# Kernel tuning notes

Hardware: AMD Instinct MI355X
Metric: run time of the kernel (lower is better)

## Reference

```python
import jax, jax.numpy as jnp
import numpy as np


def setup_inputs() -> dict:
    key = jax.random.key(0)
    k1, k2, k3, k4 = jax.random.split(key, 4)
    B, T, C = 4, 2048, 1024
    x = jax.random.normal(k1, (B, T, C), dtype=jnp.float32)
    scale = 1.0 / np.sqrt(C)
    Wq = jax.random.normal(k2, (C, C), dtype=jnp.float32) * scale
    Wk = jax.random.normal(k3, (C, C), dtype=jnp.float32) * scale
    Wv = jax.random.normal(k4, (C, C), dtype=jnp.float32) * scale
    return {"x": x, "Wq": Wq, "Wk": Wk, "Wv": Wv}


def reference(x, Wq, Wk, Wv):
    # x: [B, T, C]; torch Linear(no bias): y = x @ W.T
    B, T, C = x.shape
    q = jnp.einsum('btc,dc->btd', x, Wq)
    k = jnp.einsum('btc,dc->btd', x, Wk)
    v = jnp.einsum('btc,dc->btd', x, Wv)
    scale = jnp.asarray(C, x.dtype) ** -0.5
    qk = jnp.einsum('bqd,bkd->bqk', q, k) * scale  # [B, T, T]
    causal = jnp.tril(jnp.ones((T, T), dtype=bool))
    qk = jnp.where(causal, qk, -jnp.inf)
    attn = jax.nn.softmax(qk, axis=-1)
    out = jnp.einsum('bqk,bkd->bqd', attn, v)
    return out
```

## Files before the change

### kernel.cpp

```cpp
#include <hip/hip_runtime.h>

typedef __attribute__((ext_vector_type(8))) short  short8;
typedef __attribute__((ext_vector_type(4))) short  short4v;
typedef __attribute__((ext_vector_type(4))) float  floatx4;

__device__ inline short f2bf(float f) {
    union { float f; unsigned u; } v; v.f = f;
    unsigned r = v.u + 0x7fffu + ((v.u >> 16) & 1u);
    return (short)(r >> 16);
}

typedef const __attribute__((address_space(1))) unsigned int* gp1_t;
typedef __attribute__((address_space(3))) unsigned int* lp3_t;

__device__ __attribute__((always_inline)) inline void gl_lds16(const short* g, short* l) {
    __builtin_amdgcn_global_load_lds((gp1_t)g, (lp3_t)l, 16, 0, 0);
}

#define MFMA_BF16 __builtin_amdgcn_mfma_f32_16x16x32_bf16

__device__ __attribute__((always_inline)) inline void gemm_bt_core(
    const short* __restrict__ Ag, const short* __restrict__ Bg,
    int lda, int ldb, int kmax,
    short* As, short* Bs, floatx4 acc[4][4])
{
    const int t    = threadIdx.x;
    const int srow = t >> 3;
    const int scol = (t & 7) * 8;
    const int lane = t & 63;
    const int wid  = t >> 6;
    const int wx   = wid & 1, wy = wid >> 1;
    const int lm   = lane & 15, lq = lane >> 4;

    for (int k0 = 0; k0 < kmax; k0 += 64) {
        __syncthreads();
#pragma unroll
        for (int i = 0; i < 4; ++i) {
            gl_lds16(Ag + (size_t)(i * 32 + srow) * lda + k0 + scol,
                     As + (i * 32 + srow) * 64 + scol);
            gl_lds16(Bg + (size_t)(i * 32 + srow) * ldb + k0 + scol,
                     Bs + (i * 32 + srow) * 64 + scol);
        }
        __syncthreads();

#pragma unroll
        for (int ks = 0; ks < 2; ++ks) {
            short8 af[4], bfr[4];
#pragma unroll
            for (int mi = 0; mi < 4; ++mi)
                af[mi] = *(const short8*)(As + (wy * 64 + mi * 16 + lm) * 64 + ks * 32 + lq * 8);
#pragma unroll
            for (int ni = 0; ni < 4; ++ni)
                bfr[ni] = *(const short8*)(Bs + (wx * 64 + ni * 16 + lm) * 64 + ks * 32 + lq * 8);
#pragma unroll
            for (int mi = 0; mi < 4; ++mi)
#pragma unroll
                for (int ni = 0; ni < 4; ++ni)
                    acc[mi][ni] = MFMA_BF16(af[mi], bfr[ni], acc[mi][ni], 0, 0, 0);
        }
    }
}

__global__ void cast_all(const float* __restrict__ x,
                         const float* __restrict__ Wq,
                         const float* __restrict__ Wk,
                         const float* __restrict__ Wv,
                         short* __restrict__ xb, short* __restrict__ wb,
                         float* __restrict__ lsum)
{
    size_t v = (size_t)blockIdx.x * 256 + threadIdx.x;
    const float* src; short* dst; size_t off;
    if (v < 2097152)      { src = x;  dst = xb;           off = v; }
    else if (v < 2359296) { src = Wq; dst = wb;           off = v - 2097152; }
    else if (v < 2621440) { src = Wk; dst = wb + 1048576; off = v - 2359296; }
    else if (v < 2883584) { src = Wv; dst = wb + 2097152; off = v - 2621440; }
    else if (v < 2885632) {
        floatx4 z = {0.f, 0.f, 0.f, 0.f};
        ((floatx4*)lsum)[v - 2883584] = z;
        return;
    } else return;
    floatx4 vv = ((const floatx4*)src)[off];
    short4v s;
#pragma unroll
    for (int e = 0; e < 4; ++e) s[e] = f2bf(vv[e]);
    ((short4v*)dst)[off] = s;
}

__global__ __launch_bounds__(256, 3) void qkv_gemm(
    const short* __restrict__ xb, const short* __restrict__ wb,
    short* __restrict__ qb, short* __restrict__ kb, short* __restrict__ vt)
{
    __shared__ short As[128 * 64];
    __shared__ short Bs[128 * 64];

    const int m0    = blockIdx.x * 128;
    const int which = blockIdx.y >> 3;
    const int n0    = (blockIdx.y & 7) * 128;

    floatx4 acc[4][4];
    floatx4 zero = {0.f, 0.f, 0.f, 0.f};
#pragma unroll
    for (int i = 0; i < 4; ++i)
#pragma unroll
        for (int j = 0; j < 4; ++j) acc[i][j] = zero;

    gemm_bt_core(xb + (size_t)m0 * 1024,
                 wb + (size_t)blockIdx.y * 128 * 1024,
                 1024, 1024, 1024, As, Bs, acc);

    const int lane = threadIdx.x & 63, wid = threadIdx.x >> 6;
    const int wx = wid & 1, wy = wid >> 1, lm = lane & 15, lq = lane >> 4;
#pragma unroll
    for (int mi = 0; mi < 4; ++mi)
#pragma unroll
        for (int ni = 0; ni < 4; ++ni)
#pragma unroll
            for (int r = 0; r < 4; ++r) {
                int row = m0 + wy * 64 + mi * 16 + lq * 4 + r;
                int col = n0 + wx * 64 + ni * 16 + lm;
                short bvv = f2bf(acc[mi][ni][r]);
                if (which == 2) {
                    int bb = row >> 11, tt = row & 2047;
                    vt[((size_t)bb * 1024 + col) * 2048 + tt] = bvv;
                } else if (which == 1) {
                    kb[(size_t)row * 1024 + col] = bvv;
                } else {
                    qb[(size_t)row * 1024 + col] = bvv;
                }
            }
}

__global__ __launch_bounds__(256, 3) void sqk_gemm(
    const short* __restrict__ qb, const short* __restrict__ kb,
    short* __restrict__ P, float* __restrict__ lsum)
{
    int idx = blockIdx.x;
    int i = 0;
    while ((i + 1) * (i + 2) / 2 <= idx) ++i;
    const int j = idx - i * (i + 1) / 2;
    const int b = blockIdx.y;

    __shared__ short As[128 * 64];
    __shared__ short Bs[128 * 64];

    floatx4 acc[4][4];
    floatx4 zero = {0.f, 0.f, 0.f, 0.f};
#pragma unroll
    for (int a = 0; a < 4; ++a)
#pragma unroll
        for (int c = 0; c < 4; ++c) acc[a][c] = zero;

    gemm_bt_core(qb + ((size_t)(b * 2048 + i * 128)) * 1024,
                 kb + ((size_t)(b * 2048 + j * 128)) * 1024,
                 1024, 1024, 1024, As, Bs, acc);

    const float sscl = 0.03125f * 1.44269504089f;
    const bool  diag = (i == j);
    const int lane = threadIdx.x & 63, wid = threadIdx.x >> 6;
    const int wx = wid & 1, wy = wid >> 1, lm = lane & 15, lq = lane >> 4;

#pragma unroll
    for (int mi = 0; mi < 4; ++mi)
#pragma unroll
        for (int r = 0; r < 4; ++r) {
            const int lrow = wy * 64 + mi * 16 + lq * 4 + r;
            const int grow = i * 128 + lrow;
            short* prow = P + ((size_t)b * 2048 + grow) * 2048 + j * 128;
            float rsum = 0.f;
#pragma unroll
            for (int ni = 0; ni < 4; ++ni) {
                const int lcol = wx * 64 + ni * 16 + lm;
                float p = exp2f(acc[mi][ni][r] * sscl);
                if (diag && lcol > lrow) p = 0.f;
                rsum += p;
                prow[lcol] = f2bf(p);
            }
#pragma unroll
            for (int off = 1; off < 16; off <<= 1) rsum += __shfl_xor(rsum, off);
            if (lm == 0) atomicAdd(lsum + b * 2048 + grow, rsum);
        }
}

__global__ __launch_bounds__(256, 3) void pv_gemm(
    const short* __restrict__ P, const short* __restrict__ vt,
    const float* __restrict__ lsum, float* __restrict__ out)
{
    const int x  = blockIdx.x;
    const int b  = blockIdx.y;
    const int i  = 15 - blockIdx.z;
    const int n0 = x * 128;
    const int kmax = (i + 1) * 128;

    __shared__ short As[128 * 64];
    __shared__ short Bs[128 * 64];

    const short* Ag = P  + ((size_t)b * 2048 + i * 128) * 2048;
    const short* Bg = vt + ((size_t)b * 1024 + n0) * 2048;

    floatx4 acc[4][4];
    floatx4 zero = {0.f, 0.f, 0.f, 0.f};
#pragma unroll
    for (int a = 0; a < 4; ++a)
#pragma unroll
        for (int c = 0; c < 4; ++c) acc[a][c] = zero;

    gemm_bt_core(Ag, Bg, 2048, 2048, kmax, As, Bs, acc);

    const int lane = threadIdx.x & 63, wid = threadIdx.x >> 6;
    const int wx = wid & 1, wy = wid >> 1, lm = lane & 15, lq = lane >> 4;

#pragma unroll
    for (int mi = 0; mi < 4; ++mi)
#pragma unroll
        for (int r = 0; r < 4; ++r) {
            const int grow = b * 2048 + i * 128 + wy * 64 + mi * 16 + lq * 4 + r;
            const float li = 1.0f / lsum[grow];
#pragma unroll
            for (int ni = 0; ni < 4; ++ni)
                out[(size_t)grow * 1024 + n0 + wx * 64 + ni * 16 + lm] =
                    acc[mi][ni][r] * li;
        }
}

extern "C" void kernel_launch(void* const* d_in, const int* in_sizes, int n_in,
                              void* d_out, int out_size, void* d_ws, size_t ws_size,
                              hipStream_t stream)
{
    (void)in_sizes; (void)n_in; (void)out_size; (void)ws_size;
    const float* x  = (const float*)d_in[0];
    const float* Wq = (const float*)d_in[1];
    const float* Wk = (const float*)d_in[2];
    const float* Wv = (const float*)d_in[3];
    float* out = (float*)d_out;

    char* base = (char*)d_ws;
    short* xb   = (short*)(base);
    short* wb   = (short*)(base + 16777216);
    short* qb   = (short*)(base + 23068672);
    short* kb   = (short*)(base + 39845888);
    short* vt   = (short*)(base + 56623104);
    short* P    = (short*)(base + 73400320);
    float* lsum = (float*)(base + 107954176);

    cast_all<<<11272, 256, 0, stream>>>(x, Wq, Wk, Wv, xb, wb, lsum);
    qkv_gemm<<<dim3(64, 24), 256, 0, stream>>>(xb, wb, qb, kb, vt);
    sqk_gemm<<<dim3(136, 4), 256, 0, stream>>>(qb, kb, P, lsum);
    pv_gemm<<<dim3(8, 4, 16), 256, 0, stream>>>(P, vt, lsum, out);
}
```

Before: 249.5 us.

## Split-K long causal row blocks in PV GEMM with atomic accumulation

The PV GEMM grid now splits row blocks 8-15, which have the longest causal K ranges, into two K halves, and each half atomically adds into the output. This balances work across blocks and reduces the tail caused by the long row blocks. The cast kernel is extended to zero the second half of each batch's output rows so the atomic adds start from zero. The cost is extra blocks, float atomics on half the output, and a larger zeroing pass.

Result: no change. 250.1 us (+0.3%).

```diff
diff --git a/kernel.cpp b/kernel.cpp
--- a/kernel.cpp
+++ b/kernel.cpp
@@ -66,7 +66,7 @@
                          const float* __restrict__ Wk,
                          const float* __restrict__ Wv,
                          short* __restrict__ xb, short* __restrict__ wb,
-                         float* __restrict__ lsum)
+                         float* __restrict__ lsum, float* __restrict__ out)
 {
     size_t v = (size_t)blockIdx.x * 256 + threadIdx.x;
     const float* src; short* dst; size_t off;
@@ -77,6 +77,12 @@
     else if (v < 2885632) {
         floatx4 z = {0.f, 0.f, 0.f, 0.f};
         ((floatx4*)lsum)[v - 2883584] = z;
+        return;
+    } else if (v < 3934208) {
+        size_t u = v - 2885632;
+        size_t bb = u >> 18, r = u & 262143;
+        floatx4 z = {0.f, 0.f, 0.f, 0.f};
+        ((floatx4*)out)[(bb * 2048 + 1024) * 256 + r] = z;
         return;
     } else return;
     floatx4 vv = ((const floatx4*)src)[off];
@@ -185,26 +191,37 @@
     const short* __restrict__ P, const short* __restrict__ vt,
     const float* __restrict__ lsum, float* __restrict__ out)
 {
-    const int x  = blockIdx.x;
-    const int b  = blockIdx.y;
-    const int i  = 15 - blockIdx.z;
+    const int id = blockIdx.x;
+    const int x  = blockIdx.y;
+    const int b  = blockIdx.z;
+    int i, kbeg, kend;
+    bool single;
+    if (id < 8) {
+        i = id; kbeg = 0; kend = (i + 1) * 128; single = true;
+    } else {
+        const int id2 = id - 8;
+        i = 8 + (id2 >> 1);
+        const int c = id2 & 1;
+        kbeg = c ? 1024 : 0;
+        kend = c ? (i + 1) * 128 : 1024;
+        single = false;
+    }
     const int n0 = x * 128;
-    const int kmax = (i + 1) * 128;
 
     __shared__ short As[128 * 64];
     __shared__ short Bs[128 * 64];
 
-    const short* Ag = P  + ((size_t)b * 2048 + i * 128) * 2048;
-    const short* Bg = vt + ((size_t)b * 1024 + n0) * 2048;
+    const short* Ag = P  + ((size_t)b * 2048 + i * 128) * 2048 + kbeg;
+    const short* Bg = vt + ((size_t)b * 1024 + n0) * 2048 + kbeg;
 
     floatx4 acc[4][4];
     floatx4 zero = {0.f, 0.f, 0.f, 0.f};
 #pragma unroll
     for (int a = 0; a < 4; ++a)
 #pragma unroll
-        for (int c = 0; c < 4; ++c) acc[a][c] = zero;
-
-    gemm_bt_core(Ag, Bg, 2048, 2048, kmax, As, Bs, acc);
+        for (int c2 = 0; c2 < 4; ++c2) acc[a][c2] = zero;
+
+    gemm_bt_core(Ag, Bg, 2048, 2048, kend - kbeg, As, Bs, acc);
 
     const int lane = threadIdx.x & 63, wid = threadIdx.x >> 6;
     const int wx = wid & 1, wy = wid >> 1, lm = lane & 15, lq = lane >> 4;
@@ -216,9 +233,12 @@
             const int grow = b * 2048 + i * 128 + wy * 64 + mi * 16 + lq * 4 + r;
             const float li = 1.0f / lsum[grow];
 #pragma unroll
-            for (int ni = 0; ni < 4; ++ni)
-                out[(size_t)grow * 1024 + n0 + wx * 64 + ni * 16 + lm] =
-                    acc[mi][ni][r] * li;
+            for (int ni = 0; ni < 4; ++ni) {
+                float* dst = out + (size_t)grow * 1024 + n0 + wx * 64 + ni * 16 + lm;
+                const float val = acc[mi][ni][r] * li;
+                if (single) *dst = val;
+                else        atomicAdd(dst, val);
+            }
         }
 }
 
@@ -242,8 +262,8 @@
     short* P    = (short*)(base + 73400320);
     float* lsum = (float*)(base + 107954176);
 
-    cast_all<<<11272, 256, 0, stream>>>(x, Wq, Wk, Wv, xb, wb, lsum);
+    cast_all<<<15368, 256, 0, stream>>>(x, Wq, Wk, Wv, xb, wb, lsum, out);
     qkv_gemm<<<dim3(64, 24), 256, 0, stream>>>(xb, wb, qb, kb, vt);
     sqk_gemm<<<dim3(136, 4), 256, 0, stream>>>(qb, kb, P, lsum);
-    pv_gemm<<<dim3(8, 4, 16), 256, 0, stream>>>(P, vt, lsum, out);
-}
+    pv_gemm<<<dim3(24, 8, 4), 256, 0, stream>>>(P, vt, lsum, out);
+}
```
